# Optimization experiments

Hardware: AMD Instinct MI355X
Metric: run time of the kernel (lower is better)

Reference implementation:

```python
import jax, jax.numpy as jnp
import numpy as np

B, S, DK = 32, 2048, 64

def setup_inputs() -> dict:
    key = jax.random.key(0)
    kq, kk, kv = jax.random.split(key, 3)
    Q = jax.random.normal(kq, (B, S, DK), dtype=jnp.float32)
    K = jax.random.normal(kk, (B, S, DK), dtype=jnp.float32)
    V = jax.random.normal(kv, (B, S, DK), dtype=jnp.float32)
    return {"Q": Q, "K": K, "V": V}

def reference(Q, K, V):
    # attn_scores = Q K^T / sqrt(d_k); full [B,S,S] probs materialized (naive, non-flash)
    d_k = Q.shape[-1]
    scores = jnp.einsum('bqd,bkd->bqk', Q, K) / jnp.sqrt(jnp.asarray(d_k, Q.dtype))
    probs = jax.nn.softmax(scores, axis=-1)
    return jnp.einsum('bqk,bkd->bqd', probs, V)
```

## Files before the change

kernel.cpp:

```cpp
#include <hip/hip_runtime.h>
#include <hip/hip_bf16.h>

#define BATCH 32
#define SEQ   2048
#define DKK   64

constexpr int QT  = 128;
constexpr int KT  = 128;
constexpr int NIT = SEQ / KT;
constexpr int LSK = 66;
constexpr int LSV = 130;

typedef __attribute__((ext_vector_type(8)))  short bf16x8;
typedef __attribute__((ext_vector_type(16))) float f32x16;
typedef __attribute__((ext_vector_type(2)))  unsigned uint2v;

__device__ __forceinline__ unsigned cvt2(float a, float b) {
    union { __hip_bfloat162 h; unsigned u; } c;
    c.h = __float22bfloat162_rn(make_float2(a, b));
    return c.u;
}

__device__ __forceinline__ unsigned short b16u(float x) {
    union { __hip_bfloat16 h; unsigned short u; } t;
    t.h = __float2bfloat16(x);
    return t.u;
}

__device__ __forceinline__ float fast_exp2(float x) {
#if __has_builtin(__builtin_amdgcn_exp2f)
    return __builtin_amdgcn_exp2f(x);
#else
    return exp2f(x);
#endif
}

__global__ __launch_bounds__(256) void prep_kv(
        const float* __restrict__ K, const float* __restrict__ V,
        unsigned short* __restrict__ K16, unsigned short* __restrict__ V16) {
    __shared__ unsigned short T[64][66];
    const int b   = blockIdx.y;
    const int k0  = blockIdx.x << 6;
    const int tid = threadIdx.x;
    const int r   = tid >> 2;
    const int c   = (tid & 3) << 4;

    {
        const float* kp = K + ((size_t)b * SEQ + k0 + r) * DKK + c;
        float4 a0 = *(const float4*)(kp + 0);
        float4 a1 = *(const float4*)(kp + 4);
        float4 a2 = *(const float4*)(kp + 8);
        float4 a3 = *(const float4*)(kp + 12);
        union { bf16x8 v; unsigned u[4]; } w0, w1;
        w0.u[0] = cvt2(a0.x, a0.y); w0.u[1] = cvt2(a0.z, a0.w);
        w0.u[2] = cvt2(a1.x, a1.y); w0.u[3] = cvt2(a1.z, a1.w);
        w1.u[0] = cvt2(a2.x, a2.y); w1.u[1] = cvt2(a2.z, a2.w);
        w1.u[2] = cvt2(a3.x, a3.y); w1.u[3] = cvt2(a3.z, a3.w);
        unsigned short* kd = K16 + ((size_t)b * SEQ + k0 + r) * DKK + c;
        *(bf16x8*)(kd)     = w0.v;
        *(bf16x8*)(kd + 8) = w1.v;
    }
    {
        const float* vp = V + ((size_t)b * SEQ + k0 + r) * DKK + c;
        float4 a0 = *(const float4*)(vp + 0);
        float4 a1 = *(const float4*)(vp + 4);
        float4 a2 = *(const float4*)(vp + 8);
        float4 a3 = *(const float4*)(vp + 12);
        const float f[16] = {a0.x,a0.y,a0.z,a0.w, a1.x,a1.y,a1.z,a1.w,
                             a2.x,a2.y,a2.z,a2.w, a3.x,a3.y,a3.z,a3.w};
        #pragma unroll
        for (int j = 0; j < 16; ++j) T[c + j][r] = b16u(f[j]);
        __syncthreads();
        unsigned short* vd = V16 + ((size_t)b * DKK + r) * SEQ + k0 + c;
        union { bf16x8 v; unsigned short s[8]; } o0, o1;
        #pragma unroll
        for (int j = 0; j < 8; ++j) { o0.s[j] = T[r][c + j]; o1.s[j] = T[r][c + 8 + j]; }
        *(bf16x8*)(vd)     = o0.v;
        *(bf16x8*)(vd + 8) = o1.v;
    }
}

__global__ __launch_bounds__(256, 2) void attn_fwd(
        const float* __restrict__ Q, const unsigned short* __restrict__ K16,
        const unsigned short* __restrict__ V16, float* __restrict__ O) {
    __shared__ short Kb[2][KT][LSK];
    __shared__ short Vt[2][DKK][LSV];

    const int tid  = threadIdx.x;
    const int w    = tid >> 6;
    const int lane = tid & 63;
    const int hi   = lane >> 5;
    const int l31  = lane & 31;

    const int lin  = (int)blockIdx.x + ((int)blockIdx.y << 4);
    const int work = ((lin & 7) << 6) | (lin >> 3);
    const int b    = work >> 4;
    const int q0   = (work & 15) * QT + w * 32;

    const float qscale = 0.125f * 1.44269504088896340736f;
    bf16x8 qfrag[4];
    #pragma unroll
    for (int c = 0; c < 4; ++c) {
        const float* qp = Q + ((size_t)b * SEQ + q0 + l31) * DKK + 16*c + 8*hi;
        float4 a  = *(const float4*)qp;
        float4 a2 = *(const float4*)(qp + 4);
        union { bf16x8 v; unsigned u[4]; } f;
        f.u[0] = cvt2(a.x*qscale,  a.y*qscale);
        f.u[1] = cvt2(a.z*qscale,  a.w*qscale);
        f.u[2] = cvt2(a2.x*qscale, a2.y*qscale);
        f.u[3] = cvt2(a2.z*qscale, a2.w*qscale);
        qfrag[c] = f.v;
    }

    f32x16 o0 = {}, o1 = {};
    float ls0 = 0.f, ls1 = 0.f, ls2 = 0.f, ls3 = 0.f;

    const unsigned short* Kbase = K16 + (size_t)b * SEQ * DKK;
    const unsigned short* Vbase = V16 + (size_t)b * DKK * SEQ;

    const int sr = tid >> 3;
    const int sc = (tid & 7) << 3;

    bf16x8 kreg[4], vreg[4];
    auto load_regs = [&](int t) {
        const unsigned short* Kg = Kbase + (size_t)(t * KT) * DKK + sc;
        #pragma unroll
        for (int i = 0; i < 4; ++i)
            kreg[i] = *(const bf16x8*)(Kg + (size_t)(sr + 32*i) * DKK);
        const unsigned short* Vg = Vbase + (size_t)sr * SEQ + t * KT + sc;
        #pragma unroll
        for (int i = 0; i < 2; ++i) {
            vreg[2*i]     = *(const bf16x8*)(Vg + (size_t)(32*i) * SEQ);
            vreg[2*i + 1] = *(const bf16x8*)(Vg + (size_t)(32*i) * SEQ + 64);
        }
    };
    auto write_lds = [&](int buf) {
        #pragma unroll
        for (int i = 0; i < 4; ++i)
            *(bf16x8*)&Kb[buf][sr + 32*i][sc] = kreg[i];
        #pragma unroll
        for (int i = 0; i < 2; ++i) {
            *(bf16x8*)&Vt[buf][sr + 32*i][sc]      = vreg[2*i];
            *(bf16x8*)&Vt[buf][sr + 32*i][sc + 64] = vreg[2*i + 1];
        }
    };

    load_regs(0);
    write_lds(0);
    load_regs(1);
    __syncthreads();

    for (int it = 0; it < NIT; ++it) {
        const int cur = it & 1;

        #pragma unroll
        for (int kt2 = 0; kt2 < 4; ++kt2) {
            f32x16 acc = {};
            __builtin_amdgcn_s_setprio(1);
            #pragma unroll
            for (int cd = 0; cd < 4; ++cd) {
                bf16x8 kf = *(const bf16x8*)&Kb[cur][32*kt2 + l31][16*cd + 8*hi];
                acc = __builtin_amdgcn_mfma_f32_32x32x16_bf16(kf, qfrag[cd], acc, 0, 0, 0);
            }
            __builtin_amdgcn_s_setprio(0);

            float p[16];
            #pragma unroll
            for (int r = 0; r < 16; r += 4) {
                p[r]   = fast_exp2(acc[r]);   ls0 += p[r];
                p[r+1] = fast_exp2(acc[r+1]); ls1 += p[r+1];
                p[r+2] = fast_exp2(acc[r+2]); ls2 += p[r+2];
                p[r+3] = fast_exp2(acc[r+3]); ls3 += p[r+3];
            }

            unsigned pw0 = cvt2(p[0],  p[1]),  pw1 = cvt2(p[2],  p[3]);
            unsigned pw2 = cvt2(p[4],  p[5]),  pw3 = cvt2(p[6],  p[7]);
            unsigned pw4 = cvt2(p[8],  p[9]),  pw5 = cvt2(p[10], p[11]);
            unsigned pw6 = cvt2(p[12], p[13]), pw7 = cvt2(p[14], p[15]);
            uint2v s02 = __builtin_amdgcn_permlane32_swap(pw0, pw2, false, false);
            uint2v s13 = __builtin_amdgcn_permlane32_swap(pw1, pw3, false, false);
            uint2v s46 = __builtin_amdgcn_permlane32_swap(pw4, pw6, false, false);
            uint2v s57 = __builtin_amdgcn_permlane32_swap(pw5, pw7, false, false);
            union { bf16x8 v; unsigned u[4]; } pa0, pa1;
            pa0.u[0] = s02[0]; pa0.u[1] = s13[0]; pa0.u[2] = s02[1]; pa0.u[3] = s13[1];
            pa1.u[0] = s46[0]; pa1.u[1] = s57[0]; pa1.u[2] = s46[1]; pa1.u[3] = s57[1];

            __builtin_amdgcn_s_setprio(1);
            #pragma unroll
            for (int cc = 0; cc < 2; ++cc) {
                const int c = 2*kt2 + cc;
                bf16x8 pf  = cc ? pa1.v : pa0.v;
                bf16x8 vf0 = *(const bf16x8*)&Vt[cur][l31     ][16*c + 8*hi];
                bf16x8 vf1 = *(const bf16x8*)&Vt[cur][32 + l31][16*c + 8*hi];
                o0 = __builtin_amdgcn_mfma_f32_32x32x16_bf16(vf0, pf, o0, 0, 0, 0);
                o1 = __builtin_amdgcn_mfma_f32_32x32x16_bf16(vf1, pf, o1, 0, 0, 0);
            }
            __builtin_amdgcn_s_setprio(0);
        }

        if (it + 1 < NIT) {
            write_lds(1 - cur);
            if (it + 2 < NIT) load_regs(it + 2);
            asm volatile("s_waitcnt lgkmcnt(0)" ::: "memory");
            __builtin_amdgcn_s_barrier();
        }
    }

    float s = (ls0 + ls1) + (ls2 + ls3);
    s += __shfl_xor(s, 32);
    const float inv = 1.0f / s;

    float* op = O + ((size_t)b * SEQ + q0 + l31) * DKK;
    #pragma unroll
    for (int G = 0; G < 4; ++G) {
        float4 st;
        st.x = o0[4*G + 0] * inv; st.y = o0[4*G + 1] * inv;
        st.z = o0[4*G + 2] * inv; st.w = o0[4*G + 3] * inv;
        *(float4*)(op + 8*G + 4*hi) = st;
        st.x = o1[4*G + 0] * inv; st.y = o1[4*G + 1] * inv;
        st.z = o1[4*G + 2] * inv; st.w = o1[4*G + 3] * inv;
        *(float4*)(op + 32 + 8*G + 4*hi) = st;
    }
}

extern "C" void kernel_launch(void* const* d_in, const int* in_sizes, int n_in,
                              void* d_out, int out_size, void* d_ws, size_t ws_size,
                              hipStream_t stream) {
    const float* Q = (const float*)d_in[0];
    const float* K = (const float*)d_in[1];
    const float* V = (const float*)d_in[2];
    float* O = (float*)d_out;

    unsigned short* K16 = (unsigned short*)d_ws;
    unsigned short* V16 = K16 + (size_t)BATCH * SEQ * DKK;

    prep_kv<<<dim3(SEQ / 64, BATCH), dim3(256), 0, stream>>>(K, V, K16, V16);
    dim3 grid(SEQ / QT, BATCH);
    attn_fwd<<<grid, dim3(256), 0, stream>>>(Q, K16, V16, O);
}
```

Measured before the change: 137.6 us.

## Software-pipeline QK and PV MFMA stages across sub-tiles within each K tile

Restructures the inner loop over four 32-key sub-tiles so the QK^T MFMA for the next sub-tile is issued before the exp/pack/PV of the current one, using two score accumulators and preloaded V fragments. The aim is to overlap transcendental and permute work with matrix-core execution and hide LDS latency. It also drops the s_setprio hints. The cost is extra registers for the second accumulator and the V fragment arrays, which could lower occupancy.

```diff
diff --git a/kernel.cpp b/kernel.cpp
--- a/kernel.cpp
+++ b/kernel.cpp
@@ -153,17 +153,24 @@
     for (int it = 0; it < NIT; ++it) {
         const int cur = it & 1;
 
-        #pragma unroll
-        for (int kt2 = 0; kt2 < 4; ++kt2) {
-            f32x16 acc = {};
-            __builtin_amdgcn_s_setprio(1);
+        auto qk = [&](int n) {
+            f32x16 a = {};
             #pragma unroll
             for (int cd = 0; cd < 4; ++cd) {
-                bf16x8 kf = *(const bf16x8*)&Kb[cur][32*kt2 + l31][16*cd + 8*hi];
-                acc = __builtin_amdgcn_mfma_f32_32x32x16_bf16(kf, qfrag[cd], acc, 0, 0, 0);
+                bf16x8 kf = *(const bf16x8*)&Kb[cur][32*n + l31][16*cd + 8*hi];
+                a = __builtin_amdgcn_mfma_f32_32x32x16_bf16(kf, qfrag[cd], a, 0, 0, 0);
             }
-            __builtin_amdgcn_s_setprio(0);
-
+            return a;
+        };
+        auto ldvf = [&](int n, bf16x8* vf) {
+            #pragma unroll
+            for (int cc = 0; cc < 2; ++cc) {
+                const int c = 2*n + cc;
+                vf[2*cc]     = *(const bf16x8*)&Vt[cur][l31     ][16*c + 8*hi];
+                vf[2*cc + 1] = *(const bf16x8*)&Vt[cur][32 + l31][16*c + 8*hi];
+            }
+        };
+        auto smpack = [&](const f32x16& acc, bf16x8& pa0v, bf16x8& pa1v) {
             float p[16];
             #pragma unroll
             for (int r = 0; r < 16; r += 4) {
@@ -172,7 +179,6 @@
                 p[r+2] = fast_exp2(acc[r+2]); ls2 += p[r+2];
                 p[r+3] = fast_exp2(acc[r+3]); ls3 += p[r+3];
             }
-
             unsigned pw0 = cvt2(p[0],  p[1]),  pw1 = cvt2(p[2],  p[3]);
             unsigned pw2 = cvt2(p[4],  p[5]),  pw3 = cvt2(p[6],  p[7]);
             unsigned pw4 = cvt2(p[8],  p[9]),  pw5 = cvt2(p[10], p[11]);
@@ -184,19 +190,26 @@
             union { bf16x8 v; unsigned u[4]; } pa0, pa1;
             pa0.u[0] = s02[0]; pa0.u[1] = s13[0]; pa0.u[2] = s02[1]; pa0.u[3] = s13[1];
             pa1.u[0] = s46[0]; pa1.u[1] = s57[0]; pa1.u[2] = s46[1]; pa1.u[3] = s57[1];
-
-            __builtin_amdgcn_s_setprio(1);
-            #pragma unroll
-            for (int cc = 0; cc < 2; ++cc) {
-                const int c = 2*kt2 + cc;
-                bf16x8 pf  = cc ? pa1.v : pa0.v;
-                bf16x8 vf0 = *(const bf16x8*)&Vt[cur][l31     ][16*c + 8*hi];
-                bf16x8 vf1 = *(const bf16x8*)&Vt[cur][32 + l31][16*c + 8*hi];
-                o0 = __builtin_amdgcn_mfma_f32_32x32x16_bf16(vf0, pf, o0, 0, 0, 0);
-                o1 = __builtin_amdgcn_mfma_f32_32x32x16_bf16(vf1, pf, o1, 0, 0, 0);
-            }
-            __builtin_amdgcn_s_setprio(0);
-        }
+            pa0v = pa0.v; pa1v = pa1.v;
+        };
+        auto pv = [&](bf16x8 pa0v, bf16x8 pa1v, const bf16x8* vf) {
+            o0 = __builtin_amdgcn_mfma_f32_32x32x16_bf16(vf[0], pa0v, o0, 0, 0, 0);
+            o1 = __builtin_amdgcn_mfma_f32_32x32x16_bf16(vf[1], pa0v, o1, 0, 0, 0);
+            o0 = __builtin_amdgcn_mfma_f32_32x32x16_bf16(vf[2], pa1v, o0, 0, 0, 0);
+            o1 = __builtin_amdgcn_mfma_f32_32x32x16_bf16(vf[3], pa1v, o1, 0, 0, 0);
+        };
+
+        f32x16 accA, accB;
+        bf16x8 vA[4], vB[4], pa0, pa1;
+
+        accA = qk(0); ldvf(0, vA);
+        accB = qk(1); ldvf(1, vB);
+        smpack(accA, pa0, pa1); pv(pa0, pa1, vA);
+        accA = qk(2); ldvf(2, vA);
+        smpack(accB, pa0, pa1); pv(pa0, pa1, vB);
+        accB = qk(3); ldvf(3, vB);
+        smpack(accA, pa0, pa1); pv(pa0, pa1, vA);
+        smpack(accB, pa0, pa1); pv(pa0, pa1, vB);
 
         if (it + 1 < NIT) {
             write_lds(1 - cur);
```

New measurement: 138.8 us. Within noise of the previous version (+0.9%).
